# Optimization experiments

Hardware: AMD Instinct MI355X
Metric: run time of the kernel (lower is better)

The kernel has to match this reference:

```python
import jax, jax.numpy as jnp
import numpy as np

DROPOUT_P = 0.5  # pre-softmax dropout prob from __init__
_MASK_KEY = jax.random.key(42)  # fixed key -> deterministic dropout mask


def setup_inputs() -> dict:
    key = jax.random.key(0)
    kq, kk, kv = jax.random.split(key, 3)
    shape = (4, 16, 1024, 64)  # [B, H, S, D]
    Q = jax.random.normal(kq, shape, dtype=jnp.float32)
    K = jax.random.normal(kk, shape, dtype=jnp.float32)
    V = jax.random.normal(kv, shape, dtype=jnp.float32)
    return {"Q": Q, "K": K, "V": V}


def reference(Q, K, V):
    # scores: [B, H, S, S] = Q @ K^T  (no 1/sqrt(d) scaling: scale=False)
    scores = jnp.einsum("bhqd,bhkd->bhqk", Q, K)
    # pre-softmax dropout (train mode, p=0.5), deterministic fixed-key mask
    keep = jax.random.bernoulli(_MASK_KEY, 1.0 - DROPOUT_P, scores.shape)
    scores = jnp.where(keep, scores / (1.0 - DROPOUT_P), 0.0)
    attn = jax.nn.softmax(scores, axis=-1)
    return jnp.einsum("bhqk,bhkd->bhqd", attn, V)
```

## Files before the change

kernel.cpp:

```cpp
#include <hip/hip_runtime.h>
#include <hip/hip_bf16.h>
#include <hip/hip_fp16.h>

typedef _Float16 f16x8 __attribute__((ext_vector_type(8)));
typedef float f32x4 __attribute__((ext_vector_type(4)));

#define S_LEN 1024
#define DH 64
#define KVB 64
#define NIT (S_LEN / KVB)
#define PAD 8
#define ROWE (64 + PAD)

__device__ __forceinline__ unsigned rotl(unsigned x, unsigned r) {
  return (x << r) | (x >> (32u - r));
}

__device__ __forceinline__ bool keep_bit(unsigned e) {
  const unsigned ks1 = 42u;
  const unsigned ks2 = 0x1BD11BF0u;
  unsigned x0 = 0u;
  unsigned x1 = e + ks1;
#define TFR(Ra,Rb,Rc,Rd) \
  x0 += x1; x1 = rotl(x1, Ra); x1 ^= x0; \
  x0 += x1; x1 = rotl(x1, Rb); x1 ^= x0; \
  x0 += x1; x1 = rotl(x1, Rc); x1 ^= x0; \
  x0 += x1; x1 = rotl(x1, Rd); x1 ^= x0;
  TFR(13u,15u,26u, 6u)  x0 += ks1; x1 += ks2 + 1u;
  TFR(17u,29u,16u,24u)  x0 += ks2; x1 += 2u;
  TFR(13u,15u,26u, 6u)   x1 += ks1 + 3u;
  TFR(17u,29u,16u,24u)  x0 += ks1; x1 += ks2 + 4u;
  TFR(13u,15u,26u, 6u)  x0 += ks2; x1 += 5u;
#undef TFR
  return ((x0 ^ x1) >> 31) == 0u;
}

__global__ __launch_bounds__(256)
void attn_dropout_kernel(const float* __restrict__ Q, const float* __restrict__ K,
                         const float* __restrict__ V, float* __restrict__ out) {
  __shared__ _Float16 Kl[KVB][ROWE];
  __shared__ _Float16 Vt[DH][ROWE];
  __shared__ _Float16 Pl[4][16][ROWE];

  const unsigned bh   = blockIdx.x >> 4;
  const unsigned q0   = (blockIdx.x & 15u) * 64u;
  const unsigned tid  = threadIdx.x;
  const unsigned w    = tid >> 6;
  const unsigned lane = tid & 63u;
  const unsigned g    = lane >> 4;
  const unsigned ln   = lane & 15u;
  const unsigned qw   = q0 + w * 16u;

  f16x8 Qa0, Qa1;
  {
    const float* Qp = Q + (size_t)(bh * S_LEN + qw + ln) * DH + g * 8;
    f32x4 a = *(const f32x4*)(Qp);
    f32x4 b = *(const f32x4*)(Qp + 4);
    f32x4 c = *(const f32x4*)(Qp + 32);
    f32x4 d = *(const f32x4*)(Qp + 36);
#pragma unroll
    for (int i = 0; i < 4; ++i) {
      Qa0[i] = (_Float16)a[i]; Qa0[4 + i] = (_Float16)b[i];
      Qa1[i] = (_Float16)c[i]; Qa1[4 + i] = (_Float16)d[i];
    }
  }

  float mrun[4], lrun[4];
  f32x4 accO[4];
#pragma unroll
  for (int r = 0; r < 4; ++r) { mrun[r] = -1e30f; lrun[r] = 0.0f; }
#pragma unroll
  for (int n = 0; n < 4; ++n) accO[n] = (f32x4){0.f, 0.f, 0.f, 0.f};

  const unsigned kk = tid >> 2;
  const unsigned dg = tid & 3u;

  for (int t = 0; t < NIT; ++t) {
    __syncthreads();
    {
      const float* Kp = K + (size_t)(bh * S_LEN + t * KVB + kk) * DH + dg * 16;
      f32x4 k0 = *(const f32x4*)(Kp);
      f32x4 k1 = *(const f32x4*)(Kp + 4);
      f32x4 k2 = *(const f32x4*)(Kp + 8);
      f32x4 k3 = *(const f32x4*)(Kp + 12);
      f16x8 w0, w1;
#pragma unroll
      for (int i = 0; i < 4; ++i) {
        w0[i] = (_Float16)k0[i]; w0[4 + i] = (_Float16)k1[i];
        w1[i] = (_Float16)k2[i]; w1[4 + i] = (_Float16)k3[i];
      }
      *(f16x8*)&Kl[kk][dg * 16]     = w0;
      *(f16x8*)&Kl[kk][dg * 16 + 8] = w1;
    }
    {
      const float* Vp = V + (size_t)(bh * S_LEN + t * KVB + kk) * DH + dg * 16;
      f32x4 v0 = *(const f32x4*)(Vp);
      f32x4 v1 = *(const f32x4*)(Vp + 4);
      f32x4 v2 = *(const f32x4*)(Vp + 8);
      f32x4 v3 = *(const f32x4*)(Vp + 12);
#pragma unroll
      for (int i = 0; i < 4; ++i) {
        Vt[dg * 16 +  0 + i][kk] = (_Float16)v0[i];
        Vt[dg * 16 +  4 + i][kk] = (_Float16)v1[i];
        Vt[dg * 16 +  8 + i][kk] = (_Float16)v2[i];
        Vt[dg * 16 + 12 + i][kk] = (_Float16)v3[i];
      }
    }
    __syncthreads();

    f32x4 sc[4];
#pragma unroll
    for (int nt = 0; nt < 4; ++nt) {
      f16x8 kb0 = *(const f16x8*)&Kl[nt * 16 + ln][g * 8];
      f16x8 kb1 = *(const f16x8*)&Kl[nt * 16 + ln][32 + g * 8];
      f32x4 a = (f32x4){0.f, 0.f, 0.f, 0.f};
      a = __builtin_amdgcn_mfma_f32_16x16x32_f16(Qa0, kb0, a, 0, 0, 0);
      a = __builtin_amdgcn_mfma_f32_16x16x32_f16(Qa1, kb1, a, 0, 0, 0);
      sc[nt] = a;
    }

    float sm[4][4];
#pragma unroll
    for (int nt = 0; nt < 4; ++nt) {
#pragma unroll
      for (int r = 0; r < 4; ++r) {
        unsigned q  = qw + g * 4 + r;
        unsigned kg = (unsigned)t * KVB + nt * 16 + ln;
        unsigned e  = (bh << 20) + (q << 10) + kg;
        float s2 = sc[nt][r] * 2.0f;
        sm[nt][r] = keep_bit(e) ? s2 : 0.0f;
      }
    }

    float ps[4][4];
#pragma unroll
    for (int r = 0; r < 4; ++r) {
      float mx = fmaxf(fmaxf(sm[0][r], sm[1][r]), fmaxf(sm[2][r], sm[3][r]));
#pragma unroll
      for (int off = 1; off < 16; off <<= 1) mx = fmaxf(mx, __shfl_xor(mx, off));
      float mn = fmaxf(mrun[r], mx);
      float scl = __expf(mrun[r] - mn);
      mrun[r] = mn;
      float rs = 0.f;
#pragma unroll
      for (int nt = 0; nt < 4; ++nt) {
        float p = __expf(sm[nt][r] - mn);
        ps[nt][r] = p; rs += p;
      }
#pragma unroll
      for (int off = 1; off < 16; off <<= 1) rs += __shfl_xor(rs, off);
      lrun[r] = lrun[r] * scl + rs;
#pragma unroll
      for (int n = 0; n < 4; ++n) accO[n][r] *= scl;
    }

#pragma unroll
    for (int nt = 0; nt < 4; ++nt)
#pragma unroll
      for (int r = 0; r < 4; ++r)
        Pl[w][g * 4 + r][nt * 16 + ln] = (_Float16)ps[nt][r];

    f16x8 Pa0 = *(const f16x8*)&Pl[w][ln][g * 8];
    f16x8 Pa1 = *(const f16x8*)&Pl[w][ln][32 + g * 8];
#pragma unroll
    for (int nd = 0; nd < 4; ++nd) {
      f16x8 vb0 = *(const f16x8*)&Vt[nd * 16 + ln][g * 8];
      f16x8 vb1 = *(const f16x8*)&Vt[nd * 16 + ln][32 + g * 8];
      accO[nd] = __builtin_amdgcn_mfma_f32_16x16x32_f16(Pa0, vb0, accO[nd], 0, 0, 0);
      accO[nd] = __builtin_amdgcn_mfma_f32_16x16x32_f16(Pa1, vb1, accO[nd], 0, 0, 0);
    }
  }

#pragma unroll
  for (int nd = 0; nd < 4; ++nd) {
#pragma unroll
    for (int r = 0; r < 4; ++r) {
      unsigned q = qw + g * 4 + r;
      out[(size_t)(bh * S_LEN + q) * DH + nd * 16 + ln] = accO[nd][r] / lrun[r];
    }
  }
}

extern "C" void kernel_launch(void* const* d_in, const int* in_sizes, int n_in,
                              void* d_out, int out_size, void* d_ws, size_t ws_size,
                              hipStream_t stream) {
  const float* Q = (const float*)d_in[0];
  const float* K = (const float*)d_in[1];
  const float* V = (const float*)d_in[2];
  float* out = (float*)d_out;
  dim3 grid(64 * 16);
  dim3 block(256);
  hipLaunchKernelGGL(attn_dropout_kernel, grid, block, 0, stream, Q, K, V, out);
}
```

Measured before the change: 244.6 us.

## Split each KV tile across two wave groups and merge softmax states at end

Doubles the block to 512 threads. Each group of four waves handles half of every 64-key tile, so each wave evaluates only half of the per-element Philox dropout hashes and MFMAs. The partial outputs and running max/sum from the second group are merged through shared memory at the end. It also uses packed RTZ float-to-half conversion and an alignbit-based rotate to make the hash and conversion paths cheaper. The costs are an extra reduction stage, more LDS use, and higher register pressure under 512-thread launch bounds.

```diff
diff --git a/kernel.cpp b/kernel.cpp
--- a/kernel.cpp
+++ b/kernel.cpp
@@ -3,17 +3,18 @@
 #include <hip/hip_fp16.h>
 
 typedef _Float16 f16x8 __attribute__((ext_vector_type(8)));
+typedef __fp16  h16x2 __attribute__((ext_vector_type(2)));
 typedef float f32x4 __attribute__((ext_vector_type(4)));
 
 #define S_LEN 1024
 #define DH 64
 #define KVB 64
-#define NIT (S_LEN / KVB)
-#define PAD 8
-#define ROWE (64 + PAD)
+#define NIT 16
+#define KROW 72
+#define PROW 40
 
 __device__ __forceinline__ unsigned rotl(unsigned x, unsigned r) {
-  return (x << r) | (x >> (32u - r));
+  return __builtin_amdgcn_alignbit(x, x, 32u - r);
 }
 
 __device__ __forceinline__ bool keep_bit(unsigned e) {
@@ -28,19 +29,31 @@
   x0 += x1; x1 = rotl(x1, Rd); x1 ^= x0;
   TFR(13u,15u,26u, 6u)  x0 += ks1; x1 += ks2 + 1u;
   TFR(17u,29u,16u,24u)  x0 += ks2; x1 += 2u;
-  TFR(13u,15u,26u, 6u)   x1 += ks1 + 3u;
+  TFR(13u,15u,26u, 6u)     x1 += ks1 + 3u;
   TFR(17u,29u,16u,24u)  x0 += ks1; x1 += ks2 + 4u;
   TFR(13u,15u,26u, 6u)  x0 += ks2; x1 += 5u;
 #undef TFR
   return ((x0 ^ x1) >> 31) == 0u;
 }
 
-__global__ __launch_bounds__(256)
+__device__ __forceinline__ f16x8 pk8(f32x4 a, f32x4 b) {
+  h16x2 p0 = __builtin_amdgcn_cvt_pkrtz(a[0], a[1]);
+  h16x2 p1 = __builtin_amdgcn_cvt_pkrtz(a[2], a[3]);
+  h16x2 p2 = __builtin_amdgcn_cvt_pkrtz(b[0], b[1]);
+  h16x2 p3 = __builtin_amdgcn_cvt_pkrtz(b[2], b[3]);
+  f16x8 r;
+  r[0]=(_Float16)p0[0]; r[1]=(_Float16)p0[1]; r[2]=(_Float16)p1[0]; r[3]=(_Float16)p1[1];
+  r[4]=(_Float16)p2[0]; r[5]=(_Float16)p2[1]; r[6]=(_Float16)p3[0]; r[7]=(_Float16)p3[1];
+  return r;
+}
+
+__global__ __launch_bounds__(512)
 void attn_dropout_kernel(const float* __restrict__ Q, const float* __restrict__ K,
                          const float* __restrict__ V, float* __restrict__ out) {
-  __shared__ _Float16 Kl[KVB][ROWE];
-  __shared__ _Float16 Vt[DH][ROWE];
-  __shared__ _Float16 Pl[4][16][ROWE];
+  __shared__ __align__(16) char smem[64*KROW*2*2 + 8*16*PROW*2];
+  _Float16* Kl = (_Float16*)smem;
+  _Float16* Vt = Kl + 64*KROW;
+  _Float16* Pl = Vt + 64*KROW;
 
   const unsigned bh   = blockIdx.x >> 4;
   const unsigned q0   = (blockIdx.x & 15u) * 64u;
@@ -49,20 +62,14 @@
   const unsigned lane = tid & 63u;
   const unsigned g    = lane >> 4;
   const unsigned ln   = lane & 15u;
-  const unsigned qw   = q0 + w * 16u;
+  const unsigned qw   = q0 + (w & 3u) * 16u;
+  const unsigned koff = (w >> 2) * 32u;
 
   f16x8 Qa0, Qa1;
   {
     const float* Qp = Q + (size_t)(bh * S_LEN + qw + ln) * DH + g * 8;
-    f32x4 a = *(const f32x4*)(Qp);
-    f32x4 b = *(const f32x4*)(Qp + 4);
-    f32x4 c = *(const f32x4*)(Qp + 32);
-    f32x4 d = *(const f32x4*)(Qp + 36);
-#pragma unroll
-    for (int i = 0; i < 4; ++i) {
-      Qa0[i] = (_Float16)a[i]; Qa0[4 + i] = (_Float16)b[i];
-      Qa1[i] = (_Float16)c[i]; Qa1[4 + i] = (_Float16)d[i];
-    }
+    Qa0 = pk8(*(const f32x4*)(Qp),      *(const f32x4*)(Qp + 4));
+    Qa1 = pk8(*(const f32x4*)(Qp + 32), *(const f32x4*)(Qp + 36));
   }
 
   float mrun[4], lrun[4];
@@ -72,78 +79,64 @@
 #pragma unroll
   for (int n = 0; n < 4; ++n) accO[n] = (f32x4){0.f, 0.f, 0.f, 0.f};
 
-  const unsigned kk = tid >> 2;
-  const unsigned dg = tid & 3u;
+  const unsigned kk = tid >> 3;
+  const unsigned dg = (tid & 7u) * 8u;
 
   for (int t = 0; t < NIT; ++t) {
     __syncthreads();
     {
-      const float* Kp = K + (size_t)(bh * S_LEN + t * KVB + kk) * DH + dg * 16;
-      f32x4 k0 = *(const f32x4*)(Kp);
-      f32x4 k1 = *(const f32x4*)(Kp + 4);
-      f32x4 k2 = *(const f32x4*)(Kp + 8);
-      f32x4 k3 = *(const f32x4*)(Kp + 12);
-      f16x8 w0, w1;
+      const float* Kp = K + (size_t)(bh * S_LEN + t * KVB + kk) * DH + dg;
+      *(f16x8*)&Kl[kk * KROW + dg] = pk8(*(const f32x4*)Kp, *(const f32x4*)(Kp + 4));
+    }
+    {
+      const float* Vp = V + (size_t)(bh * S_LEN + t * KVB + kk) * DH + dg;
+      f32x4 v0 = *(const f32x4*)Vp;
+      f32x4 v1 = *(const f32x4*)(Vp + 4);
 #pragma unroll
       for (int i = 0; i < 4; ++i) {
-        w0[i] = (_Float16)k0[i]; w0[4 + i] = (_Float16)k1[i];
-        w1[i] = (_Float16)k2[i]; w1[4 + i] = (_Float16)k3[i];
-      }
-      *(f16x8*)&Kl[kk][dg * 16]     = w0;
-      *(f16x8*)&Kl[kk][dg * 16 + 8] = w1;
-    }
-    {
-      const float* Vp = V + (size_t)(bh * S_LEN + t * KVB + kk) * DH + dg * 16;
-      f32x4 v0 = *(const f32x4*)(Vp);
-      f32x4 v1 = *(const f32x4*)(Vp + 4);
-      f32x4 v2 = *(const f32x4*)(Vp + 8);
-      f32x4 v3 = *(const f32x4*)(Vp + 12);
-#pragma unroll
-      for (int i = 0; i < 4; ++i) {
-        Vt[dg * 16 +  0 + i][kk] = (_Float16)v0[i];
-        Vt[dg * 16 +  4 + i][kk] = (_Float16)v1[i];
-        Vt[dg * 16 +  8 + i][kk] = (_Float16)v2[i];
-        Vt[dg * 16 + 12 + i][kk] = (_Float16)v3[i];
+        Vt[(dg + i) * KROW + kk]     = (_Float16)v0[i];
+        Vt[(dg + 4 + i) * KROW + kk] = (_Float16)v1[i];
       }
     }
     __syncthreads();
 
-    f32x4 sc[4];
-#pragma unroll
-    for (int nt = 0; nt < 4; ++nt) {
-      f16x8 kb0 = *(const f16x8*)&Kl[nt * 16 + ln][g * 8];
-      f16x8 kb1 = *(const f16x8*)&Kl[nt * 16 + ln][32 + g * 8];
+    f32x4 sc[2];
+#pragma unroll
+    for (int nt = 0; nt < 2; ++nt) {
+      const unsigned krow = koff + nt * 16 + ln;
+      f16x8 kb0 = *(const f16x8*)&Kl[krow * KROW + g * 8];
+      f16x8 kb1 = *(const f16x8*)&Kl[krow * KROW + 32 + g * 8];
       f32x4 a = (f32x4){0.f, 0.f, 0.f, 0.f};
       a = __builtin_amdgcn_mfma_f32_16x16x32_f16(Qa0, kb0, a, 0, 0, 0);
       a = __builtin_amdgcn_mfma_f32_16x16x32_f16(Qa1, kb1, a, 0, 0, 0);
       sc[nt] = a;
     }
 
-    float sm[4][4];
-#pragma unroll
-    for (int nt = 0; nt < 4; ++nt) {
+    float sm[2][4];
+#pragma unroll
+    for (int nt = 0; nt < 2; ++nt) {
 #pragma unroll
       for (int r = 0; r < 4; ++r) {
         unsigned q  = qw + g * 4 + r;
-        unsigned kg = (unsigned)t * KVB + nt * 16 + ln;
+        unsigned kg = (unsigned)t * KVB + koff + nt * 16 + ln;
         unsigned e  = (bh << 20) + (q << 10) + kg;
         float s2 = sc[nt][r] * 2.0f;
         sm[nt][r] = keep_bit(e) ? s2 : 0.0f;
       }
     }
 
-    float ps[4][4];
+    float ps[2][4];
 #pragma unroll
     for (int r = 0; r < 4; ++r) {
-      float mx = fmaxf(fmaxf(sm[0][r], sm[1][r]), fmaxf(sm[2][r], sm[3][r]));
+      float mx = fmaxf(sm[0][r], sm[1][r]);
 #pragma unroll
       for (int off = 1; off < 16; off <<= 1) mx = fmaxf(mx, __shfl_xor(mx, off));
-      float mn = fmaxf(mrun[r], mx);
+      float mn  = fmaxf(mrun[r], mx);
       float scl = __expf(mrun[r] - mn);
       mrun[r] = mn;
       float rs = 0.f;
 #pragma unroll
-      for (int nt = 0; nt < 4; ++nt) {
+      for (int nt = 0; nt < 2; ++nt) {
         float p = __expf(sm[nt][r] - mn);
         ps[nt][r] = p; rs += p;
       }
@@ -155,29 +148,58 @@
     }
 
 #pragma unroll
-    for (int nt = 0; nt < 4; ++nt)
+    for (int nt = 0; nt < 2; ++nt)
 #pragma unroll
       for (int r = 0; r < 4; ++r)
-        Pl[w][g * 4 + r][nt * 16 + ln] = (_Float16)ps[nt][r];
-
-    f16x8 Pa0 = *(const f16x8*)&Pl[w][ln][g * 8];
-    f16x8 Pa1 = *(const f16x8*)&Pl[w][ln][32 + g * 8];
+        Pl[(w * 16 + g * 4 + r) * PROW + nt * 16 + ln] = (_Float16)ps[nt][r];
+
+    f16x8 Pa = *(const f16x8*)&Pl[(w * 16 + ln) * PROW + g * 8];
 #pragma unroll
     for (int nd = 0; nd < 4; ++nd) {
-      f16x8 vb0 = *(const f16x8*)&Vt[nd * 16 + ln][g * 8];
-      f16x8 vb1 = *(const f16x8*)&Vt[nd * 16 + ln][32 + g * 8];
-      accO[nd] = __builtin_amdgcn_mfma_f32_16x16x32_f16(Pa0, vb0, accO[nd], 0, 0, 0);
-      accO[nd] = __builtin_amdgcn_mfma_f32_16x16x32_f16(Pa1, vb1, accO[nd], 0, 0, 0);
-    }
-  }
-
-#pragma unroll
-  for (int nd = 0; nd < 4; ++nd) {
+      f16x8 vb = *(const f16x8*)&Vt[(nd * 16 + ln) * KROW + koff + g * 8];
+      accO[nd] = __builtin_amdgcn_mfma_f32_16x16x32_f16(Pa, vb, accO[nd], 0, 0, 0);
+    }
+  }
+
+  float* Om = (float*)smem;
+  float* Ml = Om + 64 * 68;
+  __syncthreads();
+  if (w >= 4) {
+    const unsigned pq = (w & 3u) * 16u;
+#pragma unroll
+    for (int nd = 0; nd < 4; ++nd)
+#pragma unroll
+      for (int r = 0; r < 4; ++r)
+        Om[(pq + g * 4 + r) * 68 + nd * 16 + ln] = accO[nd][r];
+    if (ln == 0) {
+#pragma unroll
+      for (int r = 0; r < 4; ++r) {
+        Ml[(pq + g * 4 + r) * 2 + 0] = mrun[r];
+        Ml[(pq + g * 4 + r) * 2 + 1] = lrun[r];
+      }
+    }
+  }
+  __syncthreads();
+  if (w < 4) {
+    float e1[4], e2[4], lf[4];
 #pragma unroll
     for (int r = 0; r < 4; ++r) {
-      unsigned q = qw + g * 4 + r;
-      out[(size_t)(bh * S_LEN + q) * DH + nd * 16 + ln] = accO[nd][r] / lrun[r];
-    }
+      const unsigned pq = w * 16 + g * 4 + r;
+      float m2 = Ml[pq * 2 + 0];
+      float l2 = Ml[pq * 2 + 1];
+      float m  = fmaxf(mrun[r], m2);
+      e1[r] = __expf(mrun[r] - m);
+      e2[r] = __expf(m2 - m);
+      lf[r] = lrun[r] * e1[r] + l2 * e2[r];
+    }
+#pragma unroll
+    for (int nd = 0; nd < 4; ++nd)
+#pragma unroll
+      for (int r = 0; r < 4; ++r) {
+        const unsigned pq = w * 16 + g * 4 + r;
+        float o = accO[nd][r] * e1[r] + Om[pq * 68 + nd * 16 + ln] * e2[r];
+        out[(size_t)(bh * S_LEN + q0 + pq) * DH + nd * 16 + ln] = o / lf[r];
+      }
   }
 }
 
@@ -189,6 +211,6 @@
   const float* V = (const float*)d_in[2];
   float* out = (float*)d_out;
   dim3 grid(64 * 16);
-  dim3 block(256);
+  dim3 block(512);
   hipLaunchKernelGGL(attn_dropout_kernel, grid, block, 0, stream, Q, K, V, out);
 }
```

Measured after the change: 288.0 us. 17.8% more time.

## Prefetch next K/V tile into registers and fold dropout scale into Q

Applied to the files above, without the earlier changes.

Loads the next K/V tile from global memory into registers while the current tile's MFMA and softmax work runs, so load latency overlaps compute instead of sitting between the two barriers. It also folds the 1/(1-p)=2 dropout scale into Q before the fp16 conversion, uses packed round-toward-zero fp16 conversions, and uses alignbit for the Philox rotations. This costs extra registers per thread, which may reduce occupancy. The RTZ conversion also changes rounding slightly compared with the previous round-to-nearest conversion.

```diff
diff --git a/kernel.cpp b/kernel.cpp
--- a/kernel.cpp
+++ b/kernel.cpp
@@ -3,17 +3,17 @@
 #include <hip/hip_fp16.h>
 
 typedef _Float16 f16x8 __attribute__((ext_vector_type(8)));
+typedef __fp16  h16x2 __attribute__((ext_vector_type(2)));
 typedef float f32x4 __attribute__((ext_vector_type(4)));
 
 #define S_LEN 1024
 #define DH 64
 #define KVB 64
-#define NIT (S_LEN / KVB)
-#define PAD 8
-#define ROWE (64 + PAD)
+#define NIT 16
+#define KROW 72
 
 __device__ __forceinline__ unsigned rotl(unsigned x, unsigned r) {
-  return (x << r) | (x >> (32u - r));
+  return __builtin_amdgcn_alignbit(x, x, 32u - r);
 }
 
 __device__ __forceinline__ bool keep_bit(unsigned e) {
@@ -28,19 +28,30 @@
   x0 += x1; x1 = rotl(x1, Rd); x1 ^= x0;
   TFR(13u,15u,26u, 6u)  x0 += ks1; x1 += ks2 + 1u;
   TFR(17u,29u,16u,24u)  x0 += ks2; x1 += 2u;
-  TFR(13u,15u,26u, 6u)   x1 += ks1 + 3u;
+  TFR(13u,15u,26u, 6u)     x1 += ks1 + 3u;
   TFR(17u,29u,16u,24u)  x0 += ks1; x1 += ks2 + 4u;
   TFR(13u,15u,26u, 6u)  x0 += ks2; x1 += 5u;
 #undef TFR
   return ((x0 ^ x1) >> 31) == 0u;
 }
 
+__device__ __forceinline__ f16x8 pk8(f32x4 a, f32x4 b) {
+  h16x2 p0 = __builtin_amdgcn_cvt_pkrtz(a[0], a[1]);
+  h16x2 p1 = __builtin_amdgcn_cvt_pkrtz(a[2], a[3]);
+  h16x2 p2 = __builtin_amdgcn_cvt_pkrtz(b[0], b[1]);
+  h16x2 p3 = __builtin_amdgcn_cvt_pkrtz(b[2], b[3]);
+  f16x8 r;
+  r[0]=(_Float16)p0[0]; r[1]=(_Float16)p0[1]; r[2]=(_Float16)p1[0]; r[3]=(_Float16)p1[1];
+  r[4]=(_Float16)p2[0]; r[5]=(_Float16)p2[1]; r[6]=(_Float16)p3[0]; r[7]=(_Float16)p3[1];
+  return r;
+}
+
 __global__ __launch_bounds__(256)
 void attn_dropout_kernel(const float* __restrict__ Q, const float* __restrict__ K,
                          const float* __restrict__ V, float* __restrict__ out) {
-  __shared__ _Float16 Kl[KVB][ROWE];
-  __shared__ _Float16 Vt[DH][ROWE];
-  __shared__ _Float16 Pl[4][16][ROWE];
+  __shared__ _Float16 Kl[KVB][KROW];
+  __shared__ _Float16 Vt[DH][KROW];
+  __shared__ _Float16 Pl[4][16][KROW];
 
   const unsigned bh   = blockIdx.x >> 4;
   const unsigned q0   = (blockIdx.x & 15u) * 64u;
@@ -54,15 +65,12 @@
   f16x8 Qa0, Qa1;
   {
     const float* Qp = Q + (size_t)(bh * S_LEN + qw + ln) * DH + g * 8;
-    f32x4 a = *(const f32x4*)(Qp);
-    f32x4 b = *(const f32x4*)(Qp + 4);
-    f32x4 c = *(const f32x4*)(Qp + 32);
-    f32x4 d = *(const f32x4*)(Qp + 36);
-#pragma unroll
-    for (int i = 0; i < 4; ++i) {
-      Qa0[i] = (_Float16)a[i]; Qa0[4 + i] = (_Float16)b[i];
-      Qa1[i] = (_Float16)c[i]; Qa1[4 + i] = (_Float16)d[i];
-    }
+    f32x4 a = *(const f32x4*)(Qp)      * 2.0f;
+    f32x4 b = *(const f32x4*)(Qp + 4)  * 2.0f;
+    f32x4 c = *(const f32x4*)(Qp + 32) * 2.0f;
+    f32x4 d = *(const f32x4*)(Qp + 36) * 2.0f;
+    Qa0 = pk8(a, b);
+    Qa1 = pk8(c, d);
   }
 
   float mrun[4], lrun[4];
@@ -72,41 +80,41 @@
 #pragma unroll
   for (int n = 0; n < 4; ++n) accO[n] = (f32x4){0.f, 0.f, 0.f, 0.f};
 
-  const unsigned kk = tid >> 2;
-  const unsigned dg = tid & 3u;
+  const unsigned kk  = tid >> 2;
+  const unsigned dgf = (tid & 3u) * 16u;
+
+  f32x4 kr0, kr1, kr2, kr3, vr0, vr1, vr2, vr3;
+  {
+    const float* Kp = K + (size_t)(bh * S_LEN + kk) * DH + dgf;
+    kr0 = *(const f32x4*)(Kp);  kr1 = *(const f32x4*)(Kp + 4);
+    kr2 = *(const f32x4*)(Kp + 8); kr3 = *(const f32x4*)(Kp + 12);
+    const float* Vp = V + (size_t)(bh * S_LEN + kk) * DH + dgf;
+    vr0 = *(const f32x4*)(Vp);  vr1 = *(const f32x4*)(Vp + 4);
+    vr2 = *(const f32x4*)(Vp + 8); vr3 = *(const f32x4*)(Vp + 12);
+  }
 
   for (int t = 0; t < NIT; ++t) {
     __syncthreads();
+    *(f16x8*)&Kl[kk][dgf]     = pk8(kr0, kr1);
+    *(f16x8*)&Kl[kk][dgf + 8] = pk8(kr2, kr3);
+#pragma unroll
+    for (int i = 0; i < 4; ++i) {
+      Vt[dgf +  0 + i][kk] = (_Float16)vr0[i];
+      Vt[dgf +  4 + i][kk] = (_Float16)vr1[i];
+      Vt[dgf +  8 + i][kk] = (_Float16)vr2[i];
+      Vt[dgf + 12 + i][kk] = (_Float16)vr3[i];
+    }
+    __syncthreads();
+
     {
-      const float* Kp = K + (size_t)(bh * S_LEN + t * KVB + kk) * DH + dg * 16;
-      f32x4 k0 = *(const f32x4*)(Kp);
-      f32x4 k1 = *(const f32x4*)(Kp + 4);
-      f32x4 k2 = *(const f32x4*)(Kp + 8);
-      f32x4 k3 = *(const f32x4*)(Kp + 12);
-      f16x8 w0, w1;
-#pragma unroll
-      for (int i = 0; i < 4; ++i) {
-        w0[i] = (_Float16)k0[i]; w0[4 + i] = (_Float16)k1[i];
-        w1[i] = (_Float16)k2[i]; w1[4 + i] = (_Float16)k3[i];
-      }
-      *(f16x8*)&Kl[kk][dg * 16]     = w0;
-      *(f16x8*)&Kl[kk][dg * 16 + 8] = w1;
-    }
-    {
-      const float* Vp = V + (size_t)(bh * S_LEN + t * KVB + kk) * DH + dg * 16;
-      f32x4 v0 = *(const f32x4*)(Vp);
-      f32x4 v1 = *(const f32x4*)(Vp + 4);
-      f32x4 v2 = *(const f32x4*)(Vp + 8);
-      f32x4 v3 = *(const f32x4*)(Vp + 12);
-#pragma unroll
-      for (int i = 0; i < 4; ++i) {
-        Vt[dg * 16 +  0 + i][kk] = (_Float16)v0[i];
-        Vt[dg * 16 +  4 + i][kk] = (_Float16)v1[i];
-        Vt[dg * 16 +  8 + i][kk] = (_Float16)v2[i];
-        Vt[dg * 16 + 12 + i][kk] = (_Float16)v3[i];
-      }
-    }
-    __syncthreads();
+      int tn = (t + 1 < NIT) ? t + 1 : NIT - 1;
+      const float* Kp = K + (size_t)(bh * S_LEN + tn * KVB + kk) * DH + dgf;
+      kr0 = *(const f32x4*)(Kp);  kr1 = *(const f32x4*)(Kp + 4);
+      kr2 = *(const f32x4*)(Kp + 8); kr3 = *(const f32x4*)(Kp + 12);
+      const float* Vp = V + (size_t)(bh * S_LEN + tn * KVB + kk) * DH + dgf;
+      vr0 = *(const f32x4*)(Vp);  vr1 = *(const f32x4*)(Vp + 4);
+      vr2 = *(const f32x4*)(Vp + 8); vr3 = *(const f32x4*)(Vp + 12);
+    }
 
     f32x4 sc[4];
 #pragma unroll
@@ -127,8 +135,7 @@
         unsigned q  = qw + g * 4 + r;
         unsigned kg = (unsigned)t * KVB + nt * 16 + ln;
         unsigned e  = (bh << 20) + (q << 10) + kg;
-        float s2 = sc[nt][r] * 2.0f;
-        sm[nt][r] = keep_bit(e) ? s2 : 0.0f;
+        sm[nt][r] = keep_bit(e) ? sc[nt][r] : 0.0f;
       }
     }
 
@@ -138,7 +145,7 @@
       float mx = fmaxf(fmaxf(sm[0][r], sm[1][r]), fmaxf(sm[2][r], sm[3][r]));
 #pragma unroll
       for (int off = 1; off < 16; off <<= 1) mx = fmaxf(mx, __shfl_xor(mx, off));
-      float mn = fmaxf(mrun[r], mx);
+      float mn  = fmaxf(mrun[r], mx);
       float scl = __expf(mrun[r] - mn);
       mrun[r] = mn;
       float rs = 0.f;
```

Result: no change. 248.8 us (+1.7%).
